# Optimization experiments

Hardware: AMD Instinct MI355X
Metric: run time of the kernel (lower is better)

The kernel has to match this reference:

```python
import jax, jax.numpy as jnp
import numpy as np

IN_FEATURES = 512
OUT_FEATURES = 512
GRID_SIZE = 5
SPLINE_ORDER = 3


def setup_inputs() -> dict:
    key = jax.random.key(0)
    k1, k2 = jax.random.split(key)
    x = jax.random.normal(k1, (8192, IN_FEATURES), dtype=jnp.float32)
    coefficients = jax.random.normal(
        k2, (IN_FEATURES, OUT_FEATURES, GRID_SIZE + SPLINE_ORDER), dtype=jnp.float32) * 0.1
    h = 2.0 / GRID_SIZE
    grid = jnp.linspace(-1.0 - SPLINE_ORDER * h, 1.0 + SPLINE_ORDER * h,
                        GRID_SIZE + 2 * SPLINE_ORDER + 1, dtype=jnp.float32)
    return {"x": x, "coefficients": coefficients, "grid": grid}


def _b_splines(xn, grid, order):
    # xn: (batch, in); grid: (G + 2*order + 1,)
    xe = xn[:, :, None]  # (b, i, 1)
    # k = 0: indicator of knot intervals -> (b, i, G + 2*order)
    B = ((xe >= grid[:-1]) & (xe < grid[1:])).astype(xn.dtype)
    for k in range(1, order + 1):
        left_den = grid[k:-1] - grid[:-k - 1]
        left_den = jnp.where(left_den == 0, jnp.ones_like(left_den), left_den)
        left = (xe - grid[:-k - 1]) / left_den * B[:, :, :-1]
        right_den = grid[k + 1:] - grid[1:-k]
        right_den = jnp.where(right_den == 0, jnp.ones_like(right_den), right_den)
        right = (grid[k + 1:] - xe) / right_den * B[:, :, 1:]
        B = left + right
    return B  # (b, i, G + order)


def reference(x, coefficients, grid):
    xn = jnp.tanh(x)
    bases = _b_splines(xn, grid, SPLINE_ORDER)  # (b, i, k)
    # replaces the double python loop: sum_i sum_k bases[b,i,k] * coeff[i,o,k]
    return jnp.einsum('bik,iok->bo', bases, coefficients)
```

## Files before the change

### kernel.cpp

```cpp
#include <hip/hip_runtime.h>
#include <hip/hip_bf16.h>
#include <stdint.h>


typedef short s16x8 __attribute__((ext_vector_type(8)));
typedef float f32x4 __attribute__((ext_vector_type(4)));

#define BATCH 8192
#define IN_F  512
#define OUT_F 512
#define NB    8
#define KKTOT (IN_F * NB)
#define ROWB  (KKTOT * 2)
#define NPH   64

__device__ __forceinline__ uint32_t f2bf(float f) {
    union { float f; uint32_t u; } v; v.f = f;
    return (v.u + 0x7FFFu + ((v.u >> 16) & 1u)) >> 16;
}

__device__ __forceinline__ uint32_t bf16bits(float a) {
    __hip_bfloat16 h = __float2bfloat16(a);
    union { __hip_bfloat16 h; unsigned short u; } c; c.h = h;
    return (uint32_t)c.u;
}

__device__ __forceinline__ uint4 bspline_pack(float xraw) {
    float e  = __expf(2.0f * xraw);
    float xn = 1.0f - 2.0f / (e + 1.0f);
    float u  = __fmaf_rn(xn, 2.5f, 5.5f);
    float fj = floorf(u);
    fj = fminf(fmaxf(fj, 3.0f), 7.0f);
    float t  = u - fj;
    float omt = 1.0f - t;
    float t2 = t * t;
    float t3 = t2 * t;
    const float s = 0.16666666666666666f;
    float w0 = s * omt * omt * omt;
    float w3 = s * t3;
    float w1 = s * __fmaf_rn(3.0f, t3, __fmaf_rn(-6.0f, t2, 4.0f));
    float w2 = 1.0f - w0 - w1 - w3;
    uint64_t packed = (uint64_t)(bf16bits(w0) | (bf16bits(w1) << 16))
                    | ((uint64_t)(bf16bits(w2) | (bf16bits(w3) << 16)) << 32);
    int sh = ((int)fj - 3) * 16;
    uint64_t lo, hi;
    if (sh == 0)      { lo = packed;       hi = 0ull; }
    else if (sh < 64) { lo = packed << sh; hi = packed >> (64 - sh); }
    else              { lo = 0ull;         hi = packed; }
    return make_uint4((uint32_t)lo, (uint32_t)(lo >> 32),
                      (uint32_t)hi, (uint32_t)(hi >> 32));
}

__global__ __launch_bounds__(256)
void prep_all(const float* __restrict__ X, const float* __restrict__ C,
              unsigned short* __restrict__ BtT, unsigned short* __restrict__ Abf) {
    if (blockIdx.x < 1024) {
        int t = blockIdx.x * 256 + threadIdx.x;
        int o = t & (OUT_F - 1);
        int i = t >> 9;
        const float4* src = (const float4*)(C + ((size_t)i * OUT_F + o) * NB);
        float4 c0 = src[0];
        float4 c1 = src[1];
        uint4 val;
        val.x = f2bf(c0.x) | (f2bf(c0.y) << 16);
        val.y = f2bf(c0.z) | (f2bf(c0.w) << 16);
        val.z = f2bf(c1.x) | (f2bf(c1.y) << 16);
        val.w = f2bf(c1.z) | (f2bf(c1.w) << 16);
        *(uint4*)(BtT + (size_t)o * KKTOT + (size_t)i * NB) = val;
    } else {
        int t  = (blockIdx.x - 1024) * 256 + threadIdx.x;
        int b  = t >> 7;
        int ip = t & 127;
        float4 xv = *(const float4*)(X + (size_t)b * IN_F + ip * 4);
        uint4 p0 = bspline_pack(xv.x);
        uint4 p1 = bspline_pack(xv.y);
        uint4 p2 = bspline_pack(xv.z);
        uint4 p3 = bspline_pack(xv.w);
        unsigned short* dst = Abf + (size_t)b * KKTOT + ip * 32;
        *(uint4*)(dst)      = p0;
        *(uint4*)(dst + 8)  = p1;
        *(uint4*)(dst + 16) = p2;
        *(uint4*)(dst + 24) = p3;
    }
}

__device__ __forceinline__ void gload_lds16(const void* g, void* l) {
    __builtin_amdgcn_global_load_lds(
        (const __attribute__((address_space(1))) uint32_t*)g,
        (__attribute__((address_space(3))) uint32_t*)l, 16, 0, 0);
}

__global__ __launch_bounds__(512, 4)
void kan_gemm_mat2(const unsigned short* __restrict__ Abf,
                   const unsigned short* __restrict__ BtT,
                   float* __restrict__ Out) {
    __shared__ uint4 smem4[4096];
    char* smem = (char*)smem4;

    const int tid    = threadIdx.x;
    const int lane   = tid & 63;
    const int wv     = tid >> 6;
    const int gg     = wv >> 2;
    const int w      = wv & 3;
    const int wr     = w >> 1;
    const int wc     = w & 1;
    const int lane16 = lane & 15;
    const int quad   = lane >> 4;

    const int work = (blockIdx.x & 7) * 32 + (blockIdx.x >> 3);
    const int row0 = (work >> 2) * 128;
    const int col0 = (work & 3) * 128;

    const int Cchunk = (lane & 3) ^ ((lane >> 3) & 3);
    const int R0 = w * 32 + (lane >> 2);
    const size_t gk = (size_t)gg * 4096;
    const char* srcA0 = (const char*)Abf + (size_t)(row0 + R0) * ROWB + gk + Cchunk * 16;
    const char* srcA1 = srcA0 + (size_t)16 * ROWB;
    const char* srcB0 = (const char*)BtT + (size_t)(col0 + R0) * ROWB + gk + Cchunk * 16;
    const char* srcB1 = srcB0 + (size_t)16 * ROWB;
    const int wslot = w * 2048;

    const int sx = (quad ^ ((lane16 >> 1) & 3)) << 4;
    const int abase = (wr * 64 + lane16) * 64 + sx;
    const int bbase = (wc * 64 + lane16) * 64 + sx;

    f32x4 acc[4][4] = {};

#define STAGE(B_, T_)                                                         \
    do {                                                                      \
        const size_t toff = (size_t)(T_) * 64;                                \
        char* la = smem + (gg * 2 + (B_)) * 16384 + wslot;                    \
        gload_lds16(srcA0 + toff, la);                                        \
        gload_lds16(srcA1 + toff, la + 1024);                                 \
        gload_lds16(srcB0 + toff, la + 8192);                                 \
        gload_lds16(srcB1 + toff, la + 8192 + 1024);                          \
    } while (0)

#define TILE(B_)                                                              \
    do {                                                                      \
        const char* ab = smem + (gg * 2 + (B_)) * 16384;                      \
        const char* bb = ab + 8192;                                           \
        s16x8 af0 = *(const s16x8*)(ab + abase);                              \
        s16x8 af1 = *(const s16x8*)(ab + abase + 1024);                       \
        s16x8 af2 = *(const s16x8*)(ab + abase + 2048);                       \
        s16x8 af3 = *(const s16x8*)(ab + abase + 3072);                       \
        s16x8 bf0 = *(const s16x8*)(bb + bbase);                              \
        s16x8 bf1 = *(const s16x8*)(bb + bbase + 1024);                       \
        s16x8 bf2 = *(const s16x8*)(bb + bbase + 2048);                       \
        s16x8 bf3 = *(const s16x8*)(bb + bbase + 3072);                       \
        __builtin_amdgcn_s_setprio(1);                                        \
        acc[0][0] = __builtin_amdgcn_mfma_f32_16x16x32_bf16(af0, bf0, acc[0][0], 0, 0, 0); \
        acc[0][1] = __builtin_amdgcn_mfma_f32_16x16x32_bf16(af0, bf1, acc[0][1], 0, 0, 0); \
        acc[0][2] = __builtin_amdgcn_mfma_f32_16x16x32_bf16(af0, bf2, acc[0][2], 0, 0, 0); \
        acc[0][3] = __builtin_amdgcn_mfma_f32_16x16x32_bf16(af0, bf3, acc[0][3], 0, 0, 0); \
        acc[1][0] = __builtin_amdgcn_mfma_f32_16x16x32_bf16(af1, bf0, acc[1][0], 0, 0, 0); \
        acc[1][1] = __builtin_amdgcn_mfma_f32_16x16x32_bf16(af1, bf1, acc[1][1], 0, 0, 0); \
        acc[1][2] = __builtin_amdgcn_mfma_f32_16x16x32_bf16(af1, bf2, acc[1][2], 0, 0, 0); \
        acc[1][3] = __builtin_amdgcn_mfma_f32_16x16x32_bf16(af1, bf3, acc[1][3], 0, 0, 0); \
        acc[2][0] = __builtin_amdgcn_mfma_f32_16x16x32_bf16(af2, bf0, acc[2][0], 0, 0, 0); \
        acc[2][1] = __builtin_amdgcn_mfma_f32_16x16x32_bf16(af2, bf1, acc[2][1], 0, 0, 0); \
        acc[2][2] = __builtin_amdgcn_mfma_f32_16x16x32_bf16(af2, bf2, acc[2][2], 0, 0, 0); \
        acc[2][3] = __builtin_amdgcn_mfma_f32_16x16x32_bf16(af2, bf3, acc[2][3], 0, 0, 0); \
        acc[3][0] = __builtin_amdgcn_mfma_f32_16x16x32_bf16(af3, bf0, acc[3][0], 0, 0, 0); \
        acc[3][1] = __builtin_amdgcn_mfma_f32_16x16x32_bf16(af3, bf1, acc[3][1], 0, 0, 0); \
        acc[3][2] = __builtin_amdgcn_mfma_f32_16x16x32_bf16(af3, bf2, acc[3][2], 0, 0, 0); \
        acc[3][3] = __builtin_amdgcn_mfma_f32_16x16x32_bf16(af3, bf3, acc[3][3], 0, 0, 0); \
        __builtin_amdgcn_s_setprio(0);                                        \
    } while (0)

    STAGE(0, 0);
    STAGE(1, 1);

    for (int t = 0; t < NPH - 2; t += 2) {
        asm volatile("s_waitcnt vmcnt(4)" ::: "memory");
        __builtin_amdgcn_s_barrier();
        TILE(0);
        __builtin_amdgcn_s_barrier();
        STAGE(0, t + 2);
        asm volatile("s_waitcnt vmcnt(4)" ::: "memory");
        __builtin_amdgcn_s_barrier();
        TILE(1);
        __builtin_amdgcn_s_barrier();
        STAGE(1, t + 3);
    }
    asm volatile("s_waitcnt vmcnt(4)" ::: "memory");
    __builtin_amdgcn_s_barrier();
    TILE(0);
    asm volatile("s_waitcnt vmcnt(0)" ::: "memory");
    __builtin_amdgcn_s_barrier();
    TILE(1);
#undef TILE
#undef STAGE

    __builtin_amdgcn_s_barrier();
    f32x4* red = (f32x4*)smem + (size_t)w * 1024;
    if (gg == 1) {
        #pragma unroll
        for (int rm = 0; rm < 4; ++rm)
            #pragma unroll
            for (int cn = 0; cn < 4; ++cn)
                red[(rm * 4 + cn) * 64 + lane] = acc[rm][cn];
    }
    __builtin_amdgcn_s_barrier();
    if (gg == 0) {
        #pragma unroll
        for (int rm = 0; rm < 4; ++rm)
            #pragma unroll
            for (int cn = 0; cn < 4; ++cn)
                acc[rm][cn] += red[(rm * 4 + cn) * 64 + lane];
        #pragma unroll
        for (int rm = 0; rm < 4; ++rm) {
            const int orow = row0 + wr * 64 + rm * 16 + quad * 4;
            #pragma unroll
            for (int cn = 0; cn < 4; ++cn) {
                float* dst = Out + (size_t)orow * OUT_F
                           + col0 + wc * 64 + cn * 16 + lane16;
                #pragma unroll
                for (int r = 0; r < 4; ++r)
                    dst[(size_t)r * OUT_F] = acc[rm][cn][r];
            }
        }
    }
}

extern "C" void kernel_launch(void* const* d_in, const int* in_sizes, int n_in,
                              void* d_out, int out_size, void* d_ws, size_t ws_size,
                              hipStream_t stream) {
    const float* X  = (const float*)d_in[0];
    const float* C  = (const float*)d_in[1];
    float* Out = (float*)d_out;

    unsigned short* BtT = (unsigned short*)d_ws;
    unsigned short* Abf = (unsigned short*)((char*)d_ws + (size_t)OUT_F * KKTOT * 2);

    prep_all<<<dim3(5120), 256, 0, stream>>>(X, C, BtT, Abf);
    kan_gemm_mat2<<<dim3(256), 512, 0, stream>>>(Abf, BtT, Out);
}
```

Before: 136.1 us.

## Load B operand directly from global into registers with 4-stage A pipeline

B fragments for the MFMA are now read straight from global memory into registers, double-buffered across phases, instead of being staged through LDS. A keeps going through LDS but now uses four buffers with a single barrier per phase, and sched_barrier pins the order of loads and MFMAs. This is meant to cut LDS traffic and barrier count. In exchange it adds register pressure (launch bounds relaxed to 2) and uncoalesced per-lane global B reads that rely on cache reuse across the 4 K-groups of waves.

```diff
diff --git a/kernel.cpp b/kernel.cpp
--- a/kernel.cpp
+++ b/kernel.cpp
@@ -90,8 +90,8 @@
         (__attribute__((address_space(3))) uint32_t*)l, 16, 0, 0);
 }
 
-__global__ __launch_bounds__(512, 4)
-void kan_gemm_mat2(const unsigned short* __restrict__ Abf,
+__global__ __launch_bounds__(512, 2)
+void kan_gemm_mat3(const unsigned short* __restrict__ Abf,
                    const unsigned short* __restrict__ BtT,
                    float* __restrict__ Out) {
     __shared__ uint4 smem4[4096];
@@ -116,81 +116,103 @@
     const size_t gk = (size_t)gg * 4096;
     const char* srcA0 = (const char*)Abf + (size_t)(row0 + R0) * ROWB + gk + Cchunk * 16;
     const char* srcA1 = srcA0 + (size_t)16 * ROWB;
-    const char* srcB0 = (const char*)BtT + (size_t)(col0 + R0) * ROWB + gk + Cchunk * 16;
-    const char* srcB1 = srcB0 + (size_t)16 * ROWB;
-    const int wslot = w * 2048;
 
     const int sx = (quad ^ ((lane16 >> 1) & 3)) << 4;
     const int abase = (wr * 64 + lane16) * 64 + sx;
-    const int bbase = (wc * 64 + lane16) * 64 + sx;
+
+    const char* bbaseg = (const char*)BtT
+        + (size_t)(col0 + wc * 64 + lane16) * ROWB + gk + quad * 16;
+    const char* bp0 = bbaseg;
+    const char* bp1 = bbaseg + (size_t)16 * ROWB;
+    const char* bp2 = bbaseg + (size_t)32 * ROWB;
+    const char* bp3 = bbaseg + (size_t)48 * ROWB;
 
     f32x4 acc[4][4] = {};
-
-#define STAGE(B_, T_)                                                         \
+    s16x8 bA0, bA1, bA2, bA3;
+    s16x8 bB0, bB1, bB2, bB3;
+
+#define STAGE_A(B_, T_)                                                       \
     do {                                                                      \
         const size_t toff = (size_t)(T_) * 64;                                \
-        char* la = smem + (gg * 2 + (B_)) * 16384 + wslot;                    \
+        char* la = smem + (B_) * 16384 + gg * 8192 + w * 2048;                \
         gload_lds16(srcA0 + toff, la);                                        \
         gload_lds16(srcA1 + toff, la + 1024);                                 \
-        gload_lds16(srcB0 + toff, la + 8192);                                 \
-        gload_lds16(srcB1 + toff, la + 8192 + 1024);                          \
-    } while (0)
-
-#define TILE(B_)                                                              \
-    do {                                                                      \
-        const char* ab = smem + (gg * 2 + (B_)) * 16384;                      \
-        const char* bb = ab + 8192;                                           \
+    } while (0)
+
+#define LOADB(R0_, R1_, R2_, R3_, T_)                                         \
+    do {                                                                      \
+        const size_t toff = (size_t)(T_) * 64;                                \
+        R0_ = *(const s16x8*)(bp0 + toff);                                    \
+        R1_ = *(const s16x8*)(bp1 + toff);                                    \
+        R2_ = *(const s16x8*)(bp2 + toff);                                    \
+        R3_ = *(const s16x8*)(bp3 + toff);                                    \
+    } while (0)
+
+#define TILE(B_, F0_, F1_, F2_, F3_)                                          \
+    do {                                                                      \
+        const char* ab = smem + (B_) * 16384 + gg * 8192;                     \
         s16x8 af0 = *(const s16x8*)(ab + abase);                              \
         s16x8 af1 = *(const s16x8*)(ab + abase + 1024);                       \
         s16x8 af2 = *(const s16x8*)(ab + abase + 2048);                       \
         s16x8 af3 = *(const s16x8*)(ab + abase + 3072);                       \
-        s16x8 bf0 = *(const s16x8*)(bb + bbase);                              \
-        s16x8 bf1 = *(const s16x8*)(bb + bbase + 1024);                       \
-        s16x8 bf2 = *(const s16x8*)(bb + bbase + 2048);                       \
-        s16x8 bf3 = *(const s16x8*)(bb + bbase + 3072);                       \
         __builtin_amdgcn_s_setprio(1);                                        \
-        acc[0][0] = __builtin_amdgcn_mfma_f32_16x16x32_bf16(af0, bf0, acc[0][0], 0, 0, 0); \
-        acc[0][1] = __builtin_amdgcn_mfma_f32_16x16x32_bf16(af0, bf1, acc[0][1], 0, 0, 0); \
-        acc[0][2] = __builtin_amdgcn_mfma_f32_16x16x32_bf16(af0, bf2, acc[0][2], 0, 0, 0); \
-        acc[0][3] = __builtin_amdgcn_mfma_f32_16x16x32_bf16(af0, bf3, acc[0][3], 0, 0, 0); \
-        acc[1][0] = __builtin_amdgcn_mfma_f32_16x16x32_bf16(af1, bf0, acc[1][0], 0, 0, 0); \
-        acc[1][1] = __builtin_amdgcn_mfma_f32_16x16x32_bf16(af1, bf1, acc[1][1], 0, 0, 0); \
-        acc[1][2] = __builtin_amdgcn_mfma_f32_16x16x32_bf16(af1, bf2, acc[1][2], 0, 0, 0); \
-        acc[1][3] = __builtin_amdgcn_mfma_f32_16x16x32_bf16(af1, bf3, acc[1][3], 0, 0, 0); \
-        acc[2][0] = __builtin_amdgcn_mfma_f32_16x16x32_bf16(af2, bf0, acc[2][0], 0, 0, 0); \
-        acc[2][1] = __builtin_amdgcn_mfma_f32_16x16x32_bf16(af2, bf1, acc[2][1], 0, 0, 0); \
-        acc[2][2] = __builtin_amdgcn_mfma_f32_16x16x32_bf16(af2, bf2, acc[2][2], 0, 0, 0); \
-        acc[2][3] = __builtin_amdgcn_mfma_f32_16x16x32_bf16(af2, bf3, acc[2][3], 0, 0, 0); \
-        acc[3][0] = __builtin_amdgcn_mfma_f32_16x16x32_bf16(af3, bf0, acc[3][0], 0, 0, 0); \
-        acc[3][1] = __builtin_amdgcn_mfma_f32_16x16x32_bf16(af3, bf1, acc[3][1], 0, 0, 0); \
-        acc[3][2] = __builtin_amdgcn_mfma_f32_16x16x32_bf16(af3, bf2, acc[3][2], 0, 0, 0); \
-        acc[3][3] = __builtin_amdgcn_mfma_f32_16x16x32_bf16(af3, bf3, acc[3][3], 0, 0, 0); \
+        acc[0][0] = __builtin_amdgcn_mfma_f32_16x16x32_bf16(af0, F0_, acc[0][0], 0, 0, 0); \
+        acc[0][1] = __builtin_amdgcn_mfma_f32_16x16x32_bf16(af0, F1_, acc[0][1], 0, 0, 0); \
+        acc[0][2] = __builtin_amdgcn_mfma_f32_16x16x32_bf16(af0, F2_, acc[0][2], 0, 0, 0); \
+        acc[0][3] = __builtin_amdgcn_mfma_f32_16x16x32_bf16(af0, F3_, acc[0][3], 0, 0, 0); \
+        acc[1][0] = __builtin_amdgcn_mfma_f32_16x16x32_bf16(af1, F0_, acc[1][0], 0, 0, 0); \
+        acc[1][1] = __builtin_amdgcn_mfma_f32_16x16x32_bf16(af1, F1_, acc[1][1], 0, 0, 0); \
+        acc[1][2] = __builtin_amdgcn_mfma_f32_16x16x32_bf16(af1, F2_, acc[1][2], 0, 0, 0); \
+        acc[1][3] = __builtin_amdgcn_mfma_f32_16x16x32_bf16(af1, F3_, acc[1][3], 0, 0, 0); \
+        acc[2][0] = __builtin_amdgcn_mfma_f32_16x16x32_bf16(af2, F0_, acc[2][0], 0, 0, 0); \
+        acc[2][1] = __builtin_amdgcn_mfma_f32_16x16x32_bf16(af2, F1_, acc[2][1], 0, 0, 0); \
+        acc[2][2] = __builtin_amdgcn_mfma_f32_16x16x32_bf16(af2, F2_, acc[2][2], 0, 0, 0); \
+        acc[2][3] = __builtin_amdgcn_mfma_f32_16x16x32_bf16(af2, F3_, acc[2][3], 0, 0, 0); \
+        acc[3][0] = __builtin_amdgcn_mfma_f32_16x16x32_bf16(af3, F0_, acc[3][0], 0, 0, 0); \
+        acc[3][1] = __builtin_amdgcn_mfma_f32_16x16x32_bf16(af3, F1_, acc[3][1], 0, 0, 0); \
+        acc[3][2] = __builtin_amdgcn_mfma_f32_16x16x32_bf16(af3, F2_, acc[3][2], 0, 0, 0); \
+        acc[3][3] = __builtin_amdgcn_mfma_f32_16x16x32_bf16(af3, F3_, acc[3][3], 0, 0, 0); \
         __builtin_amdgcn_s_setprio(0);                                        \
     } while (0)
 
-    STAGE(0, 0);
-    STAGE(1, 1);
-
-    for (int t = 0; t < NPH - 2; t += 2) {
-        asm volatile("s_waitcnt vmcnt(4)" ::: "memory");
-        __builtin_amdgcn_s_barrier();
-        TILE(0);
-        __builtin_amdgcn_s_barrier();
-        STAGE(0, t + 2);
-        asm volatile("s_waitcnt vmcnt(4)" ::: "memory");
-        __builtin_amdgcn_s_barrier();
-        TILE(1);
-        __builtin_amdgcn_s_barrier();
-        STAGE(1, t + 3);
-    }
+#define PHASE(B_, SB_, T_, CUR0,CUR1,CUR2,CUR3, NXT0,NXT1,NXT2,NXT3)          \
+    do {                                                                      \
+        asm volatile("s_waitcnt vmcnt(6)" ::: "memory");                      \
+        __builtin_amdgcn_s_barrier();                                         \
+        STAGE_A(SB_, (T_) + 2);                                               \
+        LOADB(NXT0, NXT1, NXT2, NXT3, (T_) + 1);                              \
+        asm volatile("s_waitcnt vmcnt(6)" ::: "memory");                      \
+        __builtin_amdgcn_sched_barrier(0);                                    \
+        TILE(B_, CUR0, CUR1, CUR2, CUR3);                                     \
+    } while (0)
+
+    STAGE_A(0, 0);
+    STAGE_A(1, 1);
+    LOADB(bA0, bA1, bA2, bA3, 0);
+
+    for (int t = 0; t < NPH - 4; t += 4) {
+        PHASE(0, 2, t + 0, bA0,bA1,bA2,bA3, bB0,bB1,bB2,bB3);
+        PHASE(1, 3, t + 1, bB0,bB1,bB2,bB3, bA0,bA1,bA2,bA3);
+        PHASE(2, 0, t + 2, bA0,bA1,bA2,bA3, bB0,bB1,bB2,bB3);
+        PHASE(3, 1, t + 3, bB0,bB1,bB2,bB3, bA0,bA1,bA2,bA3);
+    }
+    PHASE(0, 2, 60, bA0,bA1,bA2,bA3, bB0,bB1,bB2,bB3);
+    PHASE(1, 3, 61, bB0,bB1,bB2,bB3, bA0,bA1,bA2,bA3);
+    asm volatile("s_waitcnt vmcnt(6)" ::: "memory");
+    __builtin_amdgcn_s_barrier();
+    LOADB(bB0, bB1, bB2, bB3, 63);
     asm volatile("s_waitcnt vmcnt(4)" ::: "memory");
-    __builtin_amdgcn_s_barrier();
-    TILE(0);
+    __builtin_amdgcn_sched_barrier(0);
+    TILE(2, bA0, bA1, bA2, bA3);
+    asm volatile("s_waitcnt vmcnt(4)" ::: "memory");
+    __builtin_amdgcn_s_barrier();
     asm volatile("s_waitcnt vmcnt(0)" ::: "memory");
-    __builtin_amdgcn_s_barrier();
-    TILE(1);
+    __builtin_amdgcn_sched_barrier(0);
+    TILE(3, bB0, bB1, bB2, bB3);
+#undef PHASE
 #undef TILE
-#undef STAGE
+#undef LOADB
+#undef STAGE_A
 
     __builtin_amdgcn_s_barrier();
     f32x4* red = (f32x4*)smem + (size_t)w * 1024;
@@ -234,5 +256,5 @@
     unsigned short* Abf = (unsigned short*)((char*)d_ws + (size_t)OUT_F * KKTOT * 2);
 
     prep_all<<<dim3(5120), 256, 0, stream>>>(X, C, BtT, Abf);
-    kan_gemm_mat2<<<dim3(256), 512, 0, stream>>>(Abf, BtT, Out);
-}
+    kan_gemm_mat3<<<dim3(256), 512, 0, stream>>>(Abf, BtT, Out);
+}
```

After: 174.9 us. 28.5% more time.
